# Kernel tuning notes

Measured on AMD Instinct MI355X. Metric: run time of the kernel, lower is better.

The kernel has to match this reference:

```python
import jax, jax.numpy as jnp
import numpy as np
import math

B, T, D, H = 4, 1024, 1024, 16
HD = D // H  # 64
ROPE_BASE = 10000.0


def _apply_rope(q, k):
    # q, k: [B, H, T, HD]; interleaved even/odd rotation as in RotaryEmbedding
    t_len = q.shape[2]
    half = q.shape[-1] // 2
    inv_freq = 1.0 / (ROPE_BASE ** (jnp.arange(half, dtype=jnp.float32) / half))
    freqs = jnp.arange(t_len, dtype=jnp.float32)[:, None] * inv_freq  # [T, half]
    cos = jnp.cos(freqs)
    sin = jnp.sin(freqs)

    def rot(u):
        u1 = u[..., ::2]   # even lanes
        u2 = u[..., 1::2]  # odd lanes
        e = u1 * cos - u2 * sin
        o = u2 * cos + u1 * sin
        return jnp.stack([e, o], axis=-1).reshape(u.shape)

    return rot(q), rot(k)


def _split_heads(x):
    b, t, d = x.shape
    return x.reshape(b, t, H, HD).transpose(0, 2, 1, 3)  # [B,H,T,HD]


def _mha(x, Wq, bq, Wk, bk, Wv, bv, Wo, bo, mask):
    q = _split_heads(jnp.einsum('btd,ed->bte', x, Wq) + bq)
    k = _split_heads(jnp.einsum('btd,ed->bte', x, Wk) + bk)
    v = _split_heads(jnp.einsum('btd,ed->bte', x, Wv) + bv)
    q, k = _apply_rope(q, k)
    scores = jnp.einsum('bhtd,bhsd->bhts', q.astype(jnp.float32),
                        k.astype(jnp.float32)) / math.sqrt(HD)
    scores = jnp.where(mask, scores, -jnp.inf)
    attn = jax.nn.softmax(scores, axis=-1).astype(v.dtype)
    ctx = jnp.einsum('bhts,bhsd->bhtd', attn.astype(jnp.float32),
                     v.astype(jnp.float32)).astype(v.dtype)
    ctx = ctx.transpose(0, 2, 1, 3).reshape(x.shape[0], x.shape[1], D)
    z = jnp.einsum('btd,ed->bte', ctx, Wo) + bo
    return z


def setup_inputs() -> dict:
    key = jax.random.key(0)
    ks = jax.random.split(key, 9)
    s = 0.02
    inp = {
        'x':  jax.random.normal(ks[0], (B, T, D), jnp.float32),
        'Wq': jax.random.normal(ks[1], (D, D), jnp.float32) * s,
        'bq': jax.random.normal(ks[2], (D,), jnp.float32) * s,
        'Wk': jax.random.normal(ks[3], (D, D), jnp.float32) * s,
        'bk': jax.random.normal(ks[4], (D,), jnp.float32) * s,
        'Wv': jax.random.normal(ks[5], (D, D), jnp.float32) * s,
        'bv': jax.random.normal(ks[6], (D,), jnp.float32) * s,
        'Wo': jax.random.normal(ks[7], (D, D), jnp.float32) * s,
        'bo': jax.random.normal(ks[8], (D,), jnp.float32) * s,
        'mask': jnp.tril(jnp.ones((T, T), dtype=bool))[None, None],  # causal
    }
    return inp


def reference(x, Wq, bq, Wk, bk, Wv, bv, Wo, bo, mask):
    return _mha(x, Wq, bq, Wk, bk, Wv, bv, Wo, bo, mask)
```

## Files before the change

### kernel.cpp

```cpp
#include <hip/hip_runtime.h>


#define T_SEQ 1024
#define NH    16
#define HDIM  64
#define DM    1024
#define MTOK  4096

typedef __attribute__((ext_vector_type(8))) short short8;
typedef __attribute__((ext_vector_type(4))) float f32x4;
typedef unsigned short u16;

__device__ __forceinline__ u16 f2bf(float f) {
  unsigned int u = __builtin_bit_cast(unsigned int, f);
  u += 0x7fffu + ((u >> 16) & 1u);
  return (u16)(u >> 16);
}

__device__ __forceinline__ void gll16(const void* g, void* l) {
  __builtin_amdgcn_global_load_lds(
      (const __attribute__((address_space(1))) unsigned int*)(unsigned long long)(g),
      (__attribute__((address_space(3))) unsigned int*)(unsigned int)(unsigned long long)(l),
      16, 0, 0);
}

__global__ void prep_kernel(const float* __restrict__ x,
                            const float* __restrict__ Wq, const float* __restrict__ Wk,
                            const float* __restrict__ Wv, const float* __restrict__ Wo,
                            u16* __restrict__ xb, u16* __restrict__ wall,
                            float* __restrict__ ctab, float* __restrict__ stab) {
  const int bid = blockIdx.x, tid = threadIdx.x;
  if (bid < 8192) {
    const float* src;
    u16* dst;
    int i;
    if (bid < 4096) {
      src = x; dst = xb; i = bid * 256 + tid;
    } else {
      const int w = (bid - 4096) >> 10;
      src = w == 0 ? Wq : w == 1 ? Wk : w == 2 ? Wv : Wo;
      dst = wall + (size_t)w * (DM * DM);
      i = ((bid - 4096) & 1023) * 256 + tid;
    }
    float4 f = ((const float4*)src)[i];
    unsigned long long pk = (unsigned long long)f2bf(f.x)
                          | ((unsigned long long)f2bf(f.y) << 16)
                          | ((unsigned long long)f2bf(f.z) << 32)
                          | ((unsigned long long)f2bf(f.w) << 48);
    ((unsigned long long*)dst)[i] = pk;
  } else {
    const int idx = (bid - 8192) * 256 + tid;
    const int t = idx >> 5, i = idx & 31;
    float inv = powf(10000.f, -(float)i * (1.0f / 32.0f));
    float f = (float)t * inv;
    ctab[idx] = cosf(f);
    stab[idx] = sinf(f);
  }
}

template<int BM, int BN, int AI, int BI, int MI, int NJ>
__device__ __forceinline__ void gemm_pipe2(
    const u16* __restrict__ A, const u16* __restrict__ Bw,
    int m0, int n0, u16* As, u16* Bs, f32x4 acc[MI][NJ]) {
  const int tid = threadIdx.x, lane = tid & 63, wave = tid >> 6;
  const int wr = wave >> 1, wc = wave & 1;
  const int srcswz = ((lane & 7) ^ (lane >> 3)) * 8;
  const int NT = DM / 64;

#define STAGE2(t, b)                                                         \
  do {                                                                       \
    _Pragma("unroll") for (int i = 0; i < AI; ++i) {                         \
      const int q = (wave * AI + i) * 64 + lane;                             \
      gll16(&A[(size_t)(m0 + (q >> 3)) * DM + (t) * 64 + srcswz],            \
            &As[(b) * BM * 64 + q * 8]);                                     \
    }                                                                        \
    _Pragma("unroll") for (int i = 0; i < BI; ++i) {                         \
      const int q = (wave * BI + i) * 64 + lane;                             \
      gll16(&Bw[(size_t)(n0 + (q >> 3)) * DM + (t) * 64 + srcswz],           \
            &Bs[(b) * BN * 64 + q * 8]);                                     \
    }                                                                        \
  } while (0)

  STAGE2(0, 0);
  __syncthreads();
  int buf = 0;
  const int arow0 = wr * (BM / 2) + (lane & 15);
  const int brow0 = wc * (BN / 2) + (lane & 15);
  const int c0 = (((lane >> 4)) ^ (lane & 7)) * 8;
  const int c1 = ((4 + (lane >> 4)) ^ (lane & 7)) * 8;
  for (int t = 0; t < NT; ++t) {
    if (t + 1 < NT) STAGE2(t + 1, buf ^ 1);
    short8 af[MI][2], bf[NJ][2];
#pragma unroll
    for (int i = 0; i < MI; ++i) {
      const int r = buf * BM * 64 + (arow0 + i * 16) * 64;
      af[i][0] = *(const short8*)&As[r + c0];
      af[i][1] = *(const short8*)&As[r + c1];
    }
#pragma unroll
    for (int j = 0; j < NJ; ++j) {
      const int r = buf * BN * 64 + (brow0 + j * 16) * 64;
      bf[j][0] = *(const short8*)&Bs[r + c0];
      bf[j][1] = *(const short8*)&Bs[r + c1];
    }
#pragma unroll
    for (int i = 0; i < MI; ++i)
#pragma unroll
      for (int j = 0; j < NJ; ++j) {
        acc[i][j] = __builtin_amdgcn_mfma_f32_16x16x32_bf16(af[i][0], bf[j][0], acc[i][j], 0, 0, 0);
        acc[i][j] = __builtin_amdgcn_mfma_f32_16x16x32_bf16(af[i][1], bf[j][1], acc[i][j], 0, 0, 0);
      }
    __syncthreads();
    buf ^= 1;
  }
#undef STAGE2
}

__global__ __launch_bounds__(256, 2) void qkv_kernel(
    const u16* __restrict__ xb, const u16* __restrict__ wqkv,
    const float* __restrict__ bq, const float* __restrict__ bk, const float* __restrict__ bv,
    const float* __restrict__ ctab, const float* __restrict__ stab,
    u16* __restrict__ qbuf, u16* __restrict__ kbuf, u16* __restrict__ vt) {
  __shared__ __align__(16) u16 As[2 * 128 * 64];
  __shared__ __align__(16) u16 Bs[2 * 192 * 64];
  const int m0 = blockIdx.y * 128;
  const int n0 = blockIdx.x * 192;
  f32x4 acc[4][6];
#pragma unroll
  for (int i = 0; i < 4; ++i)
#pragma unroll
    for (int j = 0; j < 6; ++j)
#pragma unroll
      for (int r = 0; r < 4; ++r) acc[i][j][r] = 0.f;
  gemm_pipe2<128, 192, 4, 6, 4, 6>(xb, wqkv, m0, n0, As, Bs, acc);

  const int lane = threadIdx.x & 63, wave = threadIdx.x >> 6;
  const int wr = wave >> 1, wc = wave & 1;
#pragma unroll
  for (int i = 0; i < 4; ++i) {
#pragma unroll
    for (int j = 0; j < 6; ++j) {
      const int e = n0 + wc * 96 + j * 16 + (lane & 15);
      const int mode = e >> 10;
      const float* bias = mode == 0 ? bq : (mode == 1 ? bk : bv);
      const float bval = bias[e & 1023];
      const int h = (e >> 6) & 15, hd = e & 63;
#pragma unroll
      for (int r = 0; r < 4; ++r) {
        const int m = m0 + wr * 64 + i * 16 + ((lane >> 4) * 4) + r;
        const int b = m >> 10, t = m & 1023;
        float v = acc[i][j][r] + bval;
        if (mode < 2) {
          float p = __shfl_xor(v, 1);
          const int fi = hd >> 1;
          const float cc = ctab[t * 32 + fi], ss = stab[t * 32 + fi];
          v = (hd & 1) ? (v * cc + p * ss) : (v * cc - p * ss);
          u16* dst = mode == 0 ? qbuf : kbuf;
          dst[(((size_t)(b * NH + h) * T_SEQ + t) << 6) + hd] = f2bf(v);
        } else {
          vt[(((size_t)(b * NH + h) * HDIM + hd) << 10) + t] = f2bf(v);
        }
      }
    }
  }
}

__global__ __launch_bounds__(256) void attn_kernel(
    const u16* __restrict__ qbuf, const u16* __restrict__ kbuf,
    const u16* __restrict__ vtb, u16* __restrict__ ctx) {
  extern __shared__ __align__(16) u16 asmem[];
  u16* Ksm = asmem;
  u16* Vsm = asmem + 16384;
  u16* Pall = asmem + 32768;
  const int bh = blockIdx.x;
  const int b = bh >> 4, h = bh & 15;
  const int tid = threadIdx.x, lane = tid & 63, wave = tid >> 6;
  const u16* Qp = qbuf + (size_t)bh * T_SEQ * HDIM;
  const u16* Kp = kbuf + (size_t)bh * T_SEQ * HDIM;
  const u16* Vp = vtb + (size_t)bh * HDIM * T_SEQ;
  u16* Pw = Pall + wave * 2048;
  const float SC = 0.18033688f;
  const int lx = lane & 7;
  const int q4 = lane >> 4;

  short8 onesf;
#pragma unroll
  for (int i = 0; i < 8; ++i) onesf[i] = (short)0x3F80;

#define STG(kvt, bb)                                                             \
  do {                                                                           \
    _Pragma("unroll") for (int l = 0; l < 4; ++l) {                              \
      const int idx = l * 256 + tid;                                             \
      const int krow = idx >> 3, kch = (idx & 7) ^ (krow & 7);                   \
      gll16(&Kp[((kvt) * 128 + krow) * 64 + kch * 8], &Ksm[(bb) * 8192 + idx * 8]); \
    }                                                                            \
    _Pragma("unroll") for (int l = 0; l < 4; ++l) {                              \
      const int idx = l * 256 + tid;                                             \
      const int vrow = idx >> 4, c16 = idx & 15;                                 \
      const int sc = (c16 & 8) | ((c16 & 7) ^ (vrow & 7));                       \
      gll16(&Vp[(size_t)vrow * T_SEQ + (kvt) * 128 + sc * 8],                    \
            &Vsm[(bb) * 8192 + idx * 8]);                                        \
    }                                                                            \
  } while (0)

  for (int phase = 0; phase < 2; ++phase) {
    const int qt = phase ? (15 - (int)blockIdx.y) : (int)blockIdx.y;
    const int q0 = qt * 64;
    const int dkv = qt >> 1;
    const int nkv = dkv + 1;
    const int qrow = q0 + wave * 16 + (lane & 15);
    const short8 qf0 = *(const short8*)&Qp[qrow * 64 + (q4 * 8)];
    const short8 qf1 = *(const short8*)&Qp[qrow * 64 + 32 + (q4 * 8)];

    f32x4 acc_o[4], accl;
    float m_r[4];
#pragma unroll
    for (int i = 0; i < 4; ++i) {
#pragma unroll
      for (int r = 0; r < 4; ++r) acc_o[i][r] = 0.f;
      accl[i] = 0.f;
      m_r[i] = -__builtin_inff();
    }

    __syncthreads();
    STG(0, 0);
    int cur = 0;

    for (int kvt = 0; kvt < nkv; ++kvt) {
      __syncthreads();
      if (kvt + 1 < nkv) STG(kvt + 1, cur ^ 1);

      const u16* Kb = Ksm + cur * 8192;
      const u16* Vb = Vsm + cur * 8192;

      f32x4 sacc[8];
#pragma unroll
      for (int cb = 0; cb < 8; ++cb) {
#pragma unroll
        for (int r = 0; r < 4; ++r) sacc[cb][r] = 0.f;
        const int krow = cb * 16 + (lane & 15);
        const short8 kf0 = *(const short8*)&Kb[krow * 64 + ((q4 ^ (krow & 7)) * 8)];
        const short8 kf1 = *(const short8*)&Kb[krow * 64 + (((4 + q4) ^ (krow & 7)) * 8)];
        sacc[cb] = __builtin_amdgcn_mfma_f32_16x16x32_bf16(qf0, kf0, sacc[cb], 0, 0, 0);
        sacc[cb] = __builtin_amdgcn_mfma_f32_16x16x32_bf16(qf1, kf1, sacc[cb], 0, 0, 0);
      }
      if (kvt == dkv) {
        const int trow_base = q0 + wave * 16 + q4 * 4;
#pragma unroll
        for (int cb = 0; cb < 8; ++cb) {
          const int scol = kvt * 128 + cb * 16 + (lane & 15);
#pragma unroll
          for (int r = 0; r < 4; ++r)
            sacc[cb][r] = (scol > trow_base + r) ? -__builtin_inff() : sacc[cb][r] * SC;
        }
      } else {
#pragma unroll
        for (int cb = 0; cb < 8; ++cb)
#pragma unroll
          for (int r = 0; r < 4; ++r) sacc[cb][r] *= SC;
      }
      float mt[4];
#pragma unroll
      for (int r = 0; r < 4; ++r) {
        mt[r] = fmaxf(fmaxf(sacc[0][r], sacc[1][r]), fmaxf(sacc[2][r], sacc[3][r]));
        mt[r] = fmaxf(mt[r], fmaxf(fmaxf(sacc[4][r], sacc[5][r]), fmaxf(sacc[6][r], sacc[7][r])));
      }
#pragma unroll
      for (int off = 1; off < 16; off <<= 1)
#pragma unroll
        for (int r = 0; r < 4; ++r) mt[r] = fmaxf(mt[r], __shfl_xor(mt[r], off));
      float sf[4];
#pragma unroll
      for (int r = 0; r < 4; ++r) {
        const float mn = fmaxf(m_r[r], mt[r]);
        sf[r] = exp2f(m_r[r] - mn);
        m_r[r] = mn;
      }
#pragma unroll
      for (int cb = 0; cb < 8; ++cb)
#pragma unroll
        for (int r = 0; r < 4; ++r) sacc[cb][r] = exp2f(sacc[cb][r] - m_r[r]);
#pragma unroll
      for (int r = 0; r < 4; ++r) accl[r] *= sf[r];
#pragma unroll
      for (int hb = 0; hb < 4; ++hb)
#pragma unroll
        for (int r = 0; r < 4; ++r) acc_o[hb][r] *= sf[r];

#pragma unroll
      for (int cb = 0; cb < 8; ++cb)
#pragma unroll
        for (int r = 0; r < 4; ++r) {
          const int prow = q4 * 4 + r;
          const int col = cb * 16 + (lane & 15);
          Pw[prow * 128 + (col & 64) + ((col & 63) ^ ((prow & 7) << 3))] = f2bf(sacc[cb][r]);
        }

      const int prr = lane & 15;
#pragma unroll
      for (int kc = 0; kc < 4; ++kc) {
        const int lc = kc * 4 + q4;
        const int pc = (lc & 8) | ((lc & 7) ^ (prr & 7));
        const short8 pf = *(const short8*)&Pw[prr * 128 + pc * 8];
        accl = __builtin_amdgcn_mfma_f32_16x16x32_bf16(pf, onesf, accl, 0, 0, 0);
#pragma unroll
        for (int hb = 0; hb < 4; ++hb) {
          const int vrow = hb * 16 + (lane & 15);
          const int vc = (lc & 8) | ((lc & 7) ^ (vrow & 7));
          const short8 vf = *(const short8*)&Vb[vrow * 128 + vc * 8];
          acc_o[hb] = __builtin_amdgcn_mfma_f32_16x16x32_bf16(pf, vf, acc_o[hb], 0, 0, 0);
        }
      }
      cur ^= 1;
    }

#pragma unroll
    for (int hb = 0; hb < 4; ++hb) {
      const int hd = hb * 16 + (lane & 15);
#pragma unroll
      for (int r = 0; r < 4; ++r) {
        const int t = q0 + wave * 16 + q4 * 4 + r;
        const float v = acc_o[hb][r] / accl[r];
        ctx[((size_t)(b * T_SEQ + t) * NH + h) * HDIM + hd] = f2bf(v);
      }
    }
  }
#undef STG
}

__global__ __launch_bounds__(256, 2) void oproj_kernel(
    const u16* __restrict__ ctx, const u16* __restrict__ Wob,
    const float* __restrict__ bo, float* __restrict__ out) {
  __shared__ __align__(16) u16 As[2 * 64 * 64];
  __shared__ __align__(16) u16 Bs[2 * 128 * 64];
  const int lin = blockIdx.x;
  const int m0 = (lin & 63) * 64;
  const int n0 = (lin >> 6) * 128;
  f32x4 acc[2][4];
#pragma unroll
  for (int i = 0; i < 2; ++i)
#pragma unroll
    for (int j = 0; j < 4; ++j)
#pragma unroll
      for (int r = 0; r < 4; ++r) acc[i][j][r] = 0.f;
  gemm_pipe2<64, 128, 2, 4, 2, 4>(ctx, Wob, m0, n0, As, Bs, acc);
  const int lane = threadIdx.x & 63, wave = threadIdx.x >> 6;
  const int wr = wave >> 1, wc = wave & 1;
#pragma unroll
  for (int i = 0; i < 2; ++i)
#pragma unroll
    for (int j = 0; j < 4; ++j) {
      const int e = n0 + wc * 64 + j * 16 + (lane & 15);
      const float bval = bo[e];
#pragma unroll
      for (int r = 0; r < 4; ++r) {
        const int m = m0 + wr * 32 + i * 16 + ((lane >> 4) * 4) + r;
        out[(size_t)m * DM + e] = acc[i][j][r] + bval;
      }
    }
}

extern "C" void kernel_launch(void* const* d_in, const int* in_sizes, int n_in,
                              void* d_out, int out_size, void* d_ws, size_t ws_size,
                              hipStream_t stream) {
  const float* x  = (const float*)d_in[0];
  const float* Wq = (const float*)d_in[1];
  const float* bq = (const float*)d_in[2];
  const float* Wk = (const float*)d_in[3];
  const float* bk = (const float*)d_in[4];
  const float* Wv = (const float*)d_in[5];
  const float* bv = (const float*)d_in[6];
  const float* Wo = (const float*)d_in[7];
  const float* bo = (const float*)d_in[8];

  char* w = (char*)d_ws;
  u16* xb   = (u16*)(w);
  u16* wall = (u16*)(w + (8ull << 20));
  u16* wob  = (u16*)(w + (14ull << 20));
  u16* qb   = (u16*)(w + (16ull << 20));
  u16* kb   = (u16*)(w + (24ull << 20));
  u16* vtb  = (u16*)(w + (32ull << 20));
  u16* ctxb = (u16*)(w + (40ull << 20));
  float* ctab = (float*)(w + (48ull << 20));
  float* stab = ctab + T_SEQ * 32;

  hipFuncSetAttribute(reinterpret_cast<const void*>(attn_kernel),
                      hipFuncAttributeMaxDynamicSharedMemorySize, 81920);

  prep_kernel<<<dim3(8192 + 128), 256, 0, stream>>>(x, Wq, Wk, Wv, Wo, xb, wall, ctab, stab);
  qkv_kernel<<<dim3(3 * DM / 192, MTOK / 128), 256, 0, stream>>>(
      xb, wall, bq, bk, bv, ctab, stab, qb, kb, vtb);
  attn_kernel<<<dim3(64, 8), 256, 81920, stream>>>(qb, kb, vtb, ctxb);
  oproj_kernel<<<dim3(512), 256, 0, stream>>>(ctxb, wob, bo, (float*)d_out);
}
```

Baseline: 105.8 us.

## Use 128-row query tiles per block with heaviest-first scheduling in attention

Each attention block now handles one 128-row query tile (two 16-row groups per wave) instead of two paired 64-row tiles, so every K/V tile staged in LDS is reused by twice as many query rows. Blocks are launched on a 1D grid ordered so the longest causal tiles start first. This cuts K/V reloads and barriers per query row. In exchange, per-wave register pressure roughly doubles and the paired-tile load balancing is replaced by ordering alone.

```diff
diff --git a/kernel.cpp b/kernel.cpp
--- a/kernel.cpp
+++ b/kernel.cpp
@@ -172,7 +172,9 @@
   u16* Ksm = asmem;
   u16* Vsm = asmem + 16384;
   u16* Pall = asmem + 32768;
-  const int bh = blockIdx.x;
+  const int lin = blockIdx.x;
+  const int s = 7 - (lin >> 6);
+  const int bh = lin & 63;
   const int b = bh >> 4, h = bh & 15;
   const int tid = threadIdx.x, lane = tid & 63, wave = tid >> 6;
   const u16* Qp = qbuf + (size_t)bh * T_SEQ * HDIM;
@@ -180,7 +182,6 @@
   const u16* Vp = vtb + (size_t)bh * HDIM * T_SEQ;
   u16* Pw = Pall + wave * 2048;
   const float SC = 0.18033688f;
-  const int lx = lane & 7;
   const int q4 = lane >> 4;
 
   short8 onesf;
@@ -203,36 +204,42 @@
     }                                                                            \
   } while (0)
 
-  for (int phase = 0; phase < 2; ++phase) {
-    const int qt = phase ? (15 - (int)blockIdx.y) : (int)blockIdx.y;
-    const int q0 = qt * 64;
-    const int dkv = qt >> 1;
-    const int nkv = dkv + 1;
-    const int qrow = q0 + wave * 16 + (lane & 15);
-    const short8 qf0 = *(const short8*)&Qp[qrow * 64 + (q4 * 8)];
-    const short8 qf1 = *(const short8*)&Qp[qrow * 64 + 32 + (q4 * 8)];
-
-    f32x4 acc_o[4], accl;
-    float m_r[4];
-#pragma unroll
-    for (int i = 0; i < 4; ++i) {
-#pragma unroll
-      for (int r = 0; r < 4; ++r) acc_o[i][r] = 0.f;
-      accl[i] = 0.f;
-      m_r[i] = -__builtin_inff();
-    }
-
+  const int q0 = s * 128;
+  const int nkv = s + 1;
+  short8 qf[2][2];
+#pragma unroll
+  for (int g = 0; g < 2; ++g) {
+    const int qrow = q0 + wave * 32 + g * 16 + (lane & 15);
+    qf[g][0] = *(const short8*)&Qp[qrow * 64 + (q4 * 8)];
+    qf[g][1] = *(const short8*)&Qp[qrow * 64 + 32 + (q4 * 8)];
+  }
+
+  f32x4 acc_o[2][4], accl[2];
+  float m_r[2][4];
+#pragma unroll
+  for (int g = 0; g < 2; ++g) {
+#pragma unroll
+    for (int i = 0; i < 4; ++i)
+#pragma unroll
+      for (int r = 0; r < 4; ++r) acc_o[g][i][r] = 0.f;
+#pragma unroll
+    for (int r = 0; r < 4; ++r) accl[g][r] = 0.f;
+#pragma unroll
+    for (int r = 0; r < 4; ++r) m_r[g][r] = -__builtin_inff();
+  }
+
+  STG(0, 0);
+  int cur = 0;
+
+  for (int kvt = 0; kvt < nkv; ++kvt) {
     __syncthreads();
-    STG(0, 0);
-    int cur = 0;
-
-    for (int kvt = 0; kvt < nkv; ++kvt) {
-      __syncthreads();
-      if (kvt + 1 < nkv) STG(kvt + 1, cur ^ 1);
-
-      const u16* Kb = Ksm + cur * 8192;
-      const u16* Vb = Vsm + cur * 8192;
-
+    if (kvt + 1 < nkv) STG(kvt + 1, cur ^ 1);
+
+    const u16* Kb = Ksm + cur * 8192;
+    const u16* Vb = Vsm + cur * 8192;
+
+#pragma unroll
+    for (int g = 0; g < 2; ++g) {
       f32x4 sacc[8];
 #pragma unroll
       for (int cb = 0; cb < 8; ++cb) {
@@ -241,11 +248,11 @@
         const int krow = cb * 16 + (lane & 15);
         const short8 kf0 = *(const short8*)&Kb[krow * 64 + ((q4 ^ (krow & 7)) * 8)];
         const short8 kf1 = *(const short8*)&Kb[krow * 64 + (((4 + q4) ^ (krow & 7)) * 8)];
-        sacc[cb] = __builtin_amdgcn_mfma_f32_16x16x32_bf16(qf0, kf0, sacc[cb], 0, 0, 0);
-        sacc[cb] = __builtin_amdgcn_mfma_f32_16x16x32_bf16(qf1, kf1, sacc[cb], 0, 0, 0);
-      }
-      if (kvt == dkv) {
-        const int trow_base = q0 + wave * 16 + q4 * 4;
+        sacc[cb] = __builtin_amdgcn_mfma_f32_16x16x32_bf16(qf[g][0], kf0, sacc[cb], 0, 0, 0);
+        sacc[cb] = __builtin_amdgcn_mfma_f32_16x16x32_bf16(qf[g][1], kf1, sacc[cb], 0, 0, 0);
+      }
+      if (kvt == s) {
+        const int trow_base = q0 + wave * 32 + g * 16 + q4 * 4;
 #pragma unroll
         for (int cb = 0; cb < 8; ++cb) {
           const int scol = kvt * 128 + cb * 16 + (lane & 15);
@@ -272,20 +279,20 @@
       float sf[4];
 #pragma unroll
       for (int r = 0; r < 4; ++r) {
-        const float mn = fmaxf(m_r[r], mt[r]);
-        sf[r] = exp2f(m_r[r] - mn);
-        m_r[r] = mn;
+        const float mn = fmaxf(m_r[g][r], mt[r]);
+        sf[r] = exp2f(m_r[g][r] - mn);
+        m_r[g][r] = mn;
       }
 #pragma unroll
       for (int cb = 0; cb < 8; ++cb)
 #pragma unroll
-        for (int r = 0; r < 4; ++r) sacc[cb][r] = exp2f(sacc[cb][r] - m_r[r]);
-#pragma unroll
-      for (int r = 0; r < 4; ++r) accl[r] *= sf[r];
+        for (int r = 0; r < 4; ++r) sacc[cb][r] = exp2f(sacc[cb][r] - m_r[g][r]);
+#pragma unroll
+      for (int r = 0; r < 4; ++r) accl[g][r] *= sf[r];
 #pragma unroll
       for (int hb = 0; hb < 4; ++hb)
 #pragma unroll
-        for (int r = 0; r < 4; ++r) acc_o[hb][r] *= sf[r];
+        for (int r = 0; r < 4; ++r) acc_o[g][hb][r] *= sf[r];
 
 #pragma unroll
       for (int cb = 0; cb < 8; ++cb)
@@ -302,29 +309,31 @@
         const int lc = kc * 4 + q4;
         const int pc = (lc & 8) | ((lc & 7) ^ (prr & 7));
         const short8 pf = *(const short8*)&Pw[prr * 128 + pc * 8];
-        accl = __builtin_amdgcn_mfma_f32_16x16x32_bf16(pf, onesf, accl, 0, 0, 0);
+        accl[g] = __builtin_amdgcn_mfma_f32_16x16x32_bf16(pf, onesf, accl[g], 0, 0, 0);
 #pragma unroll
         for (int hb = 0; hb < 4; ++hb) {
           const int vrow = hb * 16 + (lane & 15);
           const int vc = (lc & 8) | ((lc & 7) ^ (vrow & 7));
           const short8 vf = *(const short8*)&Vb[vrow * 128 + vc * 8];
-          acc_o[hb] = __builtin_amdgcn_mfma_f32_16x16x32_bf16(pf, vf, acc_o[hb], 0, 0, 0);
+          acc_o[g][hb] = __builtin_amdgcn_mfma_f32_16x16x32_bf16(pf, vf, acc_o[g][hb], 0, 0, 0);
         }
       }
-      cur ^= 1;
-    }
-
+    }
+    cur ^= 1;
+  }
+
+#pragma unroll
+  for (int g = 0; g < 2; ++g)
 #pragma unroll
     for (int hb = 0; hb < 4; ++hb) {
       const int hd = hb * 16 + (lane & 15);
 #pragma unroll
       for (int r = 0; r < 4; ++r) {
-        const int t = q0 + wave * 16 + q4 * 4 + r;
-        const float v = acc_o[hb][r] / accl[r];
+        const int t = q0 + wave * 32 + g * 16 + q4 * 4 + r;
+        const float v = acc_o[g][hb][r] / accl[g][r];
         ctx[((size_t)(b * T_SEQ + t) * NH + h) * HDIM + hd] = f2bf(v);
       }
     }
-  }
 #undef STG
 }
 
@@ -390,6 +399,6 @@
   prep_kernel<<<dim3(8192 + 128), 256, 0, stream>>>(x, Wq, Wk, Wv, Wo, xb, wall, ctab, stab);
   qkv_kernel<<<dim3(3 * DM / 192, MTOK / 128), 256, 0, stream>>>(
       xb, wall, bq, bk, bv, ctab, stab, qb, kb, vtb);
-  attn_kernel<<<dim3(64, 8), 256, 81920, stream>>>(qb, kb, vtb, ctxb);
+  attn_kernel<<<dim3(512), 256, 81920, stream>>>(qb, kb, vtb, ctxb);
   oproj_kernel<<<dim3(512), 256, 0, stream>>>(ctxb, wob, bo, (float*)d_out);
 }
```

After: 114.4 us. 1.08x slower.

## Rewrite QKV GEMM with 512-thread 128x384 tiles and ping-pong MFMA scheduling

Applied to the files above, without the earlier changes.

Replaces the 256-thread 128x192 QKV GEMM with a 512-thread, one-block-per-CU kernel computing 128x384 tiles. K-tiles are split into half-tile LDS sections and loaded with global_load_lds. The k-loop is hand-scheduled: LDS reads and next-stage loads interleave with barrier-separated MFMA groups, under explicit vmcnt waits and raised wave priority during MFMA. The goal is to overlap memory with compute and reuse each B tile across more rows. The cost is less occupancy flexibility, a grid of only 256 blocks, and fragile hand-written barrier/waitcnt logic.

```diff
diff --git a/kernel.cpp b/kernel.cpp
--- a/kernel.cpp
+++ b/kernel.cpp
@@ -58,6 +58,149 @@
   }
 }
 
+__global__ __launch_bounds__(512, 1) void qkv_kernel(
+    const u16* __restrict__ xb, const u16* __restrict__ wqkv,
+    const float* __restrict__ bq, const float* __restrict__ bk, const float* __restrict__ bv,
+    const float* __restrict__ ctab, const float* __restrict__ stab,
+    u16* __restrict__ qbuf, u16* __restrict__ kbuf, u16* __restrict__ vt) {
+  __shared__ __align__(16) u16 As[16384];
+  __shared__ __align__(16) u16 Bs[49152];
+  const int tid = threadIdx.x, lane = tid & 63, wave = tid >> 6;
+  const int wr = wave >> 2, wc = wave & 3;
+  const int q4 = lane >> 4;
+  const int lin = blockIdx.x;
+  const int m0 = (lin & 31) * 128;
+  const int n0 = (lin >> 5) * 384;
+
+  const int ar = tid >> 3, ac = (tid & 7) ^ (ar & 7);
+  const size_t aofs = (size_t)(m0 + 2 * ar + (ac >> 2)) * DM + (ac & 3) * 8;
+  const int adst = tid * 8;
+  size_t bofs[3];
+  int bdst[3];
+#pragma unroll
+  for (int l = 0; l < 3; ++l) {
+    const int idx = l * 512 + tid, br = idx >> 3, bc = (idx & 7) ^ (br & 7);
+    bofs[l] = (size_t)(n0 + 2 * br + (bc >> 2)) * DM + (bc & 3) * 8;
+    bdst[l] = idx * 8;
+  }
+  auto stgA = [&](int kt, int kh) {
+    gll16(&xb[aofs + kt * 64 + kh * 32], &As[((kt & 1) * 2 + kh) * 4096 + adst]);
+  };
+  auto stgB = [&](int kt, int kh) {
+#pragma unroll
+    for (int l = 0; l < 3; ++l)
+      gll16(&wqkv[bofs[l] + kt * 64 + kh * 32], &Bs[((kt & 1) * 2 + kh) * 12288 + bdst[l]]);
+  };
+
+  int aoff[4], boff[6];
+#pragma unroll
+  for (int i = 0; i < 4; ++i) {
+    const int m = wr * 64 + i * 16 + (lane & 15), lr = m >> 1;
+    const int pc = (((m & 1) << 2) | q4) ^ (lr & 7);
+    aoff[i] = lr * 64 + pc * 8;
+  }
+#pragma unroll
+  for (int j = 0; j < 6; ++j) {
+    const int n = wc * 96 + j * 16 + (lane & 15), lr = n >> 1;
+    const int pc = (((n & 1) << 2) | q4) ^ (lr & 7);
+    boff[j] = lr * 64 + pc * 8;
+  }
+
+  f32x4 acc[4][6];
+#pragma unroll
+  for (int i = 0; i < 4; ++i)
+#pragma unroll
+    for (int j = 0; j < 6; ++j)
+#pragma unroll
+      for (int r = 0; r < 4; ++r) acc[i][j][r] = 0.f;
+
+  short8 af[4], bf[3];
+  auto rdA = [&](int sec) {
+#pragma unroll
+    for (int i = 0; i < 4; ++i) af[i] = *(const short8*)&As[sec * 4096 + aoff[i]];
+  };
+  auto rdB = [&](int sec, int nh) {
+#pragma unroll
+    for (int j = 0; j < 3; ++j) bf[j] = *(const short8*)&Bs[sec * 12288 + boff[nh * 3 + j]];
+  };
+
+#define MM(nh)                                                                        \
+  do {                                                                                \
+    __builtin_amdgcn_s_setprio(1);                                                    \
+    _Pragma("unroll") for (int i = 0; i < 4; ++i)                                     \
+      _Pragma("unroll") for (int j = 0; j < 3; ++j)                                   \
+        acc[i][(nh) * 3 + j] = __builtin_amdgcn_mfma_f32_16x16x32_bf16(               \
+            af[i], bf[j], acc[i][(nh) * 3 + j], 0, 0, 0);                             \
+    __builtin_amdgcn_s_setprio(0);                                                    \
+  } while (0)
+#define BAR __builtin_amdgcn_s_barrier()
+#define SGB __builtin_amdgcn_sched_barrier(0)
+
+  stgA(0, 0); stgB(0, 0); stgA(0, 1); stgB(0, 1); stgA(1, 0); stgB(1, 0);
+  asm volatile("s_waitcnt vmcnt(4)" ::: "memory");
+  BAR; SGB;
+
+#pragma unroll 1
+  for (int it = 0; it < 8; ++it) {
+    const int b = 2 * it + 1, c = 2 * it + 2, d = 2 * it + 3;
+    const bool full = (it < 7);
+    rdA(0); rdB(0, 0); stgA(b, 1);
+    BAR; MM(0); BAR;
+    rdB(0, 1); stgB(b, 1);
+    BAR; MM(1); BAR;
+    rdA(1); rdB(1, 0); if (full) stgA(c, 0);
+    BAR; MM(0); BAR;
+    rdB(1, 1);
+    if (full) {
+      stgB(c, 0);
+      asm volatile("s_waitcnt vmcnt(4)" ::: "memory");
+    } else {
+      asm volatile("s_waitcnt vmcnt(0)" ::: "memory");
+    }
+    BAR; SGB; MM(1); BAR;
+    rdA(2); rdB(2, 0); if (full) stgA(c, 1);
+    BAR; MM(0); BAR;
+    rdB(2, 1); if (full) stgB(c, 1);
+    BAR; MM(1); BAR;
+    rdA(3); rdB(3, 0); if (full) stgA(d, 0);
+    BAR; MM(0); BAR;
+    rdB(3, 1); if (full) stgB(d, 0);
+    asm volatile("s_waitcnt vmcnt(4)" ::: "memory");
+    BAR; SGB; MM(1); BAR;
+  }
+#undef MM
+#undef BAR
+#undef SGB
+
+#pragma unroll
+  for (int i = 0; i < 4; ++i) {
+#pragma unroll
+    for (int j = 0; j < 6; ++j) {
+      const int e = n0 + wc * 96 + j * 16 + (lane & 15);
+      const int mode = e >> 10;
+      const float* bias = mode == 0 ? bq : (mode == 1 ? bk : bv);
+      const float bval = bias[e & 1023];
+      const int h = (e >> 6) & 15, hd = e & 63;
+#pragma unroll
+      for (int r = 0; r < 4; ++r) {
+        const int m = m0 + wr * 64 + i * 16 + q4 * 4 + r;
+        const int bb = m >> 10, t = m & 1023;
+        float v = acc[i][j][r] + bval;
+        if (mode < 2) {
+          float p = __shfl_xor(v, 1);
+          const int fi = hd >> 1;
+          const float cc = ctab[t * 32 + fi], ss = stab[t * 32 + fi];
+          v = (hd & 1) ? (v * cc + p * ss) : (v * cc - p * ss);
+          u16* dst = mode == 0 ? qbuf : kbuf;
+          dst[(((size_t)(bb * NH + h) * T_SEQ + t) << 6) + hd] = f2bf(v);
+        } else {
+          vt[(((size_t)(bb * NH + h) * HDIM + hd) << 10) + t] = f2bf(v);
+        }
+      }
+    }
+  }
+}
+
 template<int BM, int BN, int AI, int BI, int MI, int NJ>
 __device__ __forceinline__ void gemm_pipe2(
     const u16* __restrict__ A, const u16* __restrict__ Bw,
@@ -114,55 +257,6 @@
     buf ^= 1;
   }
 #undef STAGE2
-}
-
-__global__ __launch_bounds__(256, 2) void qkv_kernel(
-    const u16* __restrict__ xb, const u16* __restrict__ wqkv,
-    const float* __restrict__ bq, const float* __restrict__ bk, const float* __restrict__ bv,
-    const float* __restrict__ ctab, const float* __restrict__ stab,
-    u16* __restrict__ qbuf, u16* __restrict__ kbuf, u16* __restrict__ vt) {
-  __shared__ __align__(16) u16 As[2 * 128 * 64];
-  __shared__ __align__(16) u16 Bs[2 * 192 * 64];
-  const int m0 = blockIdx.y * 128;
-  const int n0 = blockIdx.x * 192;
-  f32x4 acc[4][6];
-#pragma unroll
-  for (int i = 0; i < 4; ++i)
-#pragma unroll
-    for (int j = 0; j < 6; ++j)
-#pragma unroll
-      for (int r = 0; r < 4; ++r) acc[i][j][r] = 0.f;
-  gemm_pipe2<128, 192, 4, 6, 4, 6>(xb, wqkv, m0, n0, As, Bs, acc);
-
-  const int lane = threadIdx.x & 63, wave = threadIdx.x >> 6;
-  const int wr = wave >> 1, wc = wave & 1;
-#pragma unroll
-  for (int i = 0; i < 4; ++i) {
-#pragma unroll
-    for (int j = 0; j < 6; ++j) {
-      const int e = n0 + wc * 96 + j * 16 + (lane & 15);
-      const int mode = e >> 10;
-      const float* bias = mode == 0 ? bq : (mode == 1 ? bk : bv);
-      const float bval = bias[e & 1023];
-      const int h = (e >> 6) & 15, hd = e & 63;
-#pragma unroll
-      for (int r = 0; r < 4; ++r) {
-        const int m = m0 + wr * 64 + i * 16 + ((lane >> 4) * 4) + r;
-        const int b = m >> 10, t = m & 1023;
-        float v = acc[i][j][r] + bval;
-        if (mode < 2) {
-          float p = __shfl_xor(v, 1);
-          const int fi = hd >> 1;
-          const float cc = ctab[t * 32 + fi], ss = stab[t * 32 + fi];
-          v = (hd & 1) ? (v * cc + p * ss) : (v * cc - p * ss);
-          u16* dst = mode == 0 ? qbuf : kbuf;
-          dst[(((size_t)(b * NH + h) * T_SEQ + t) << 6) + hd] = f2bf(v);
-        } else {
-          vt[(((size_t)(b * NH + h) * HDIM + hd) << 10) + t] = f2bf(v);
-        }
-      }
-    }
-  }
 }
 
 __global__ __launch_bounds__(256) void attn_kernel(
@@ -180,7 +274,6 @@
   const u16* Vp = vtb + (size_t)bh * HDIM * T_SEQ;
   u16* Pw = Pall + wave * 2048;
   const float SC = 0.18033688f;
-  const int lx = lane & 7;
   const int q4 = lane >> 4;
 
   short8 onesf;
@@ -388,7 +481,7 @@
                       hipFuncAttributeMaxDynamicSharedMemorySize, 81920);
 
   prep_kernel<<<dim3(8192 + 128), 256, 0, stream>>>(x, Wq, Wk, Wv, Wo, xb, wall, ctab, stab);
-  qkv_kernel<<<dim3(3 * DM / 192, MTOK / 128), 256, 0, stream>>>(
+  qkv_kernel<<<dim3(256), 512, 0, stream>>>(
       xb, wall, bq, bk, bv, ctab, stab, qb, kb, vtb);
   attn_kernel<<<dim3(64, 8), 256, 81920, stream>>>(qb, kb, vtb, ctxb);
   oproj_kernel<<<dim3(512), 256, 0, stream>>>(ctxb, wob, bo, (float*)d_out);
```

Result: slower. 112.5 us (+6.4%).
